# Performance work log

Hardware: AMD Instinct MI355X
Metric: run time of the kernel (lower is better)

## Reference

```python
import jax, jax.numpy as jnp
import numpy as np

E, T, H, I = 16, 4, 512, 1024  # expert_num, task_num, hidden_size, input_size
B = 8192


def setup_inputs() -> dict:
    key = jax.random.key(0)
    ks = jax.random.split(key, 8)
    s_i = 1.0 / np.sqrt(I)
    s_h = 1.0 / np.sqrt(H)
    return {
        "x": jax.random.normal(ks[0], (B, I), dtype=jnp.float32),
        "We": jax.random.uniform(ks[1], (E, H, I), jnp.float32, -s_i, s_i),
        "be": jax.random.uniform(ks[2], (E, H), jnp.float32, -s_i, s_i),
        "Wg": jax.random.uniform(ks[3], (T, E, I), jnp.float32, -s_i, s_i),
        "bg": jax.random.uniform(ks[4], (T, E), jnp.float32, -s_i, s_i),
        "Wf": jax.random.uniform(ks[5], (T, H), jnp.float32, -s_h, s_h),
        "bf": jax.random.uniform(ks[6], (T,), jnp.float32, -s_h, s_h),
    }


def reference(x, We, be, Wg, bg, Wf, bf):
    # expert outputs: relu(x @ We_e^T + be_e)  -> [B, E, H]
    eo = jax.nn.relu(jnp.einsum("bi,ehi->beh", x, We) + be[None])
    # gate outputs: softmax over experts        -> [B, T, E]
    g = jax.nn.softmax(jnp.einsum("bi,tei->bte", x, Wg) + bg[None], axis=-1)
    # gated combine                             -> [T, B, H]
    res = jnp.einsum("bte,beh->tbh", g, eo)
    # per-task scalar heads                     -> [T, B, 1]
    out = jnp.einsum("tbh,th->tb", res, Wf) + bf[:, None]
    return out[:, :, None]
```

## Files before the change

### kernel.cpp

```cpp
#include <hip/hip_runtime.h>
#include <hip/hip_bf16.h>
#include <stdint.h>


#define E_ 16
#define T_ 4
#define H_ 512
#define I_ 1024
#define B_ 8192
#define N_ (E_ * H_)
#define K_ I_

typedef __bf16 bf16x8 __attribute__((ext_vector_type(8)));
typedef float f32x4 __attribute__((ext_vector_type(4)));

__device__ __forceinline__ unsigned short f2bf_rne(float f) {
  unsigned int b = __float_as_uint(f);
  b += 0x7fffu + ((b >> 16) & 1u);
  return (unsigned short)(b >> 16);
}

#define N4X (B_ * K_ / 4)
#define N4W (N_ * K_ / 4)
#define N4G (64 * K_ / 4)

__global__ __launch_bounds__(256) void cvt3_kernel(const float* __restrict__ x,
                                                   const float* __restrict__ We,
                                                   const float* __restrict__ Wg,
                                                   const float* __restrict__ bfv,
                                                   unsigned short* __restrict__ xb,
                                                   unsigned short* __restrict__ wb,
                                                   unsigned short* __restrict__ wgb,
                                                   float* __restrict__ out) {
  int i = blockIdx.x * 256 + threadIdx.x;
  if (i < T_ * B_) out[i] = bfv[i >> 13];
  const float* src;
  unsigned short* dst;
  int j;
  if (i < N4X) {
    src = x; dst = xb; j = i;
  } else if (i < N4X + N4W) {
    src = We; dst = wb; j = i - N4X;
  } else if (i < N4X + N4W + N4G) {
    src = Wg; dst = wgb; j = i - (N4X + N4W);
  } else {
    return;
  }
  float4 v = reinterpret_cast<const float4*>(src)[j];
  ushort4 o;
  o.x = f2bf_rne(v.x);
  o.y = f2bf_rne(v.y);
  o.z = f2bf_rne(v.z);
  o.w = f2bf_rne(v.w);
  reinterpret_cast<ushort4*>(dst)[j] = o;
}

__device__ __forceinline__ void gld_lds16(const void* gp, void* lp) {
  __builtin_amdgcn_global_load_lds((const __attribute__((address_space(1))) void*)gp,
                                   (__attribute__((address_space(3))) void*)lp, 16, 0, 0);
}

__global__ __launch_bounds__(256) void logits_softmax_kernel(
    const unsigned short* __restrict__ A,
    const unsigned short* __restrict__ Bm,
    const float* __restrict__ bg,
    float* __restrict__ g)
{
  __shared__ struct {
    unsigned short A[128 * 32];
    unsigned short B[64 * 32];
  } st;

  const int tid = threadIdx.x;
  const int w = tid >> 6, l = tid & 63;
  const int m16 = l & 15, q = l >> 4;
  const size_t m0 = (size_t)blockIdx.x * 128;

  const int r0s = (w * 2 + 0) * 16 + (l >> 2);
  const int r1s = (w * 2 + 1) * 16 + (l >> 2);
  const int slot = l & 3;
  const int c0 = slot ^ ((r0s >> 1) & 3);
  const int c1 = slot ^ ((r1s >> 1) & 3);
  const size_t offA0 = (m0 + r0s) * K_ + c0 * 8;
  const size_t offA1 = (m0 + r1s) * K_ + c1 * 8;
  const int l0 = (w * 2 + 0) * 512;
  const int l1 = (w * 2 + 1) * 512;
  const int rBs = w * 16 + (l >> 2);
  const int cB = slot ^ ((rBs >> 1) & 3);
  const size_t offB = (size_t)rBs * K_ + cB * 8;
  const int lB = w * 512;

  const int arow = w * 32 + m16;
  const int sA = q ^ ((arow >> 1) & 3);
  const int sB = q ^ ((m16 >> 1) & 3);

  f32x4 acc[2][4] = {};

  for (int k0 = 0; k0 < K_; k0 += 32) {
    __syncthreads();
    gld_lds16(A + offA0 + k0, st.A + l0);
    gld_lds16(A + offA1 + k0, st.A + l1);
    gld_lds16(Bm + offB + k0, st.B + lB);
    __syncthreads();
    bf16x8 af[2], bfr[4];
#pragma unroll
    for (int i = 0; i < 2; ++i)
      af[i] = *reinterpret_cast<const bf16x8*>(st.A + (arow + i * 16) * 32 + sA * 8);
#pragma unroll
    for (int j = 0; j < 4; ++j)
      bfr[j] = *reinterpret_cast<const bf16x8*>(st.B + (j * 16 + m16) * 32 + sB * 8);
#pragma unroll
    for (int i = 0; i < 2; ++i)
#pragma unroll
      for (int j = 0; j < 4; ++j)
        acc[i][j] = __builtin_amdgcn_mfma_f32_16x16x32_bf16(af[i], bfr[j], acc[i][j], 0, 0, 0);
  }

  float bgv[4];
#pragma unroll
  for (int j = 0; j < 4; ++j) bgv[j] = bg[j * 16 + m16];

#pragma unroll
  for (int i = 0; i < 2; ++i) {
    float lg[4][4];
#pragma unroll
    for (int j = 0; j < 4; ++j)
#pragma unroll
      for (int r = 0; r < 4; ++r) lg[r][j] = acc[i][j][r] + bgv[j];
#pragma unroll
    for (int r = 0; r < 4; ++r) {
#pragma unroll
      for (int j = 0; j < 4; ++j) {
        float m = lg[r][j];
#pragma unroll
        for (int mask = 1; mask < 16; mask <<= 1) m = fmaxf(m, __shfl_xor(m, mask, 64));
        float ex = __expf(lg[r][j] - m);
        float s = ex;
#pragma unroll
        for (int mask = 1; mask < 16; mask <<= 1) s += __shfl_xor(s, mask, 64);
        size_t b = m0 + w * 32 + i * 16 + q * 4 + r;
        g[b * 64 + j * 16 + m16] = ex / s;
      }
    }
  }
}


extern __shared__ char smem[];

#define BARRIER()                          \
  do {                                     \
    asm volatile("" ::: "memory");         \
    __builtin_amdgcn_s_barrier();          \
    asm volatile("" ::: "memory");         \
  } while (0)
#define VMW(n) asm volatile("s_waitcnt vmcnt(" #n ")" ::: "memory")
#define LGKM0() asm volatile("s_waitcnt lgkmcnt(0)" ::: "memory")

#define STAGE4(t_)                                                             \
  do {                                                                         \
    const int bb_ = ((t_) & 3) * 32768;                                        \
    const int ko_ = (t_) * 32;                                                 \
    gld_lds16(A + baseAg + ko_, smem + bb_ + ldsW);                            \
    gld_lds16(A + baseAg + 16 * K_ + ko_, smem + bb_ + ldsW + 1024);           \
    gld_lds16(Bm + baseBg + ko_, smem + bb_ + 16384 + ldsW);                   \
    gld_lds16(Bm + baseBg + 16 * K_ + ko_, smem + bb_ + 16384 + ldsW + 1024);  \
  } while (0)

#define COMPUTE(t_)                                                                     \
  do {                                                                                  \
    const int bb_ = ((t_) & 3) * 32768;                                                 \
    bf16x8 af[8], bfr[4];                                                               \
    _Pragma("unroll") for (int i = 0; i < 8; ++i) af[i] =                               \
        *reinterpret_cast<const bf16x8*>(smem + bb_ + baseA_rd + i * 1024 + sl16);      \
    _Pragma("unroll") for (int j = 0; j < 4; ++j) bfr[j] =                              \
        *reinterpret_cast<const bf16x8*>(smem + bb_ + 16384 + baseB_rd + j * 1024 + sl16); \
    __builtin_amdgcn_s_setprio(1);                                                      \
    _Pragma("unroll") for (int i = 0; i < 8; ++i)                                       \
        _Pragma("unroll") for (int j = 0; j < 4; ++j)                                   \
            acc[i][j] = __builtin_amdgcn_mfma_f32_16x16x32_bf16(af[i], bfr[j],          \
                                                                acc[i][j], 0, 0, 0);   \
    __builtin_amdgcn_s_setprio(0);                                                      \
  } while (0)

__global__ __launch_bounds__(512, 2) void moe_main_kernel(
    const unsigned short* __restrict__ A,
    const unsigned short* __restrict__ Bm,
    const float* __restrict__ be,
    const float* __restrict__ Wf,
    const float* __restrict__ g,
    float* __restrict__ out)
{
  const int tid = threadIdx.x;
  const int w = tid >> 6, l = tid & 63;
  const int wm = w >> 2, wn = w & 3;
  const int m16 = l & 15, q = l >> 4;
  const int mb = blockIdx.x, nb = blockIdx.y;
  const size_t m0 = (size_t)mb * 256, n0 = (size_t)nb * 256;

  const int c8 = (((l & 3) ^ ((l >> 3) & 3)) * 8);
  const size_t baseAg = (m0 + w * 32 + (l >> 2)) * K_ + c8;
  const size_t baseBg = (n0 + w * 32 + (l >> 2)) * K_ + c8;
  const int ldsW = w * 2048;

  const int sl16 = (q ^ ((m16 >> 1) & 3)) * 16;
  const int baseA_rd = (wm * 128 + m16) * 64;
  const int baseB_rd = (wn * 64 + m16) * 64;

  f32x4 acc[8][4] = {};

  STAGE4(0);
  STAGE4(1);
  STAGE4(2);

#pragma unroll 1
  for (int t = 0; t < 29; ++t) {
    VMW(8);
    BARRIER();
    STAGE4(t + 3);
    COMPUTE(t);
    LGKM0();
  }
  VMW(8);
  BARRIER();
  COMPUTE(29);
  LGKM0();
  VMW(4);
  BARRIER();
  COMPUTE(30);
  LGKM0();
  VMW(0);
  BARRIER();
  COMPUTE(31);
  LGKM0();

  __syncthreads();

  float* allsums = (float*)smem;

  const int hb = (int)(n0 & 511);
  const int e_idx = (int)(n0 >> 9);

  float wfv[4][4];
#pragma unroll
  for (int t = 0; t < 4; ++t)
#pragma unroll
    for (int j = 0; j < 4; ++j)
      wfv[t][j] = Wf[t * H_ + hb + wn * 64 + j * 16 + m16];
  float bias[4];
#pragma unroll
  for (int j = 0; j < 4; ++j) bias[j] = be[n0 + wn * 64 + j * 16 + m16];

  const int b0s = m16 & 1, b1s = (m16 >> 1) & 1, b2s = (m16 >> 2) & 1, b3s = (m16 >> 3) & 1;
#pragma unroll
  for (int i = 0; i < 8; ++i) {
    float eo[4][4];
#pragma unroll
    for (int j = 0; j < 4; ++j)
#pragma unroll
      for (int r = 0; r < 4; ++r) eo[j][r] = fmaxf(acc[i][j][r] + bias[j], 0.f);
    float p[16];
#pragma unroll
    for (int r = 0; r < 4; ++r)
#pragma unroll
      for (int t = 0; t < 4; ++t) {
        float v = 0.f;
#pragma unroll
        for (int j = 0; j < 4; ++j) v += eo[j][r] * wfv[t][j];
        p[r * 4 + t] = v;
      }
    float q8[8];
#pragma unroll
    for (int m = 0; m < 8; ++m) {
      float sent = b0s ? p[2 * m] : p[2 * m + 1];
      float recv = __shfl_xor(sent, 1, 64);
      q8[m] = (b0s ? p[2 * m + 1] : p[2 * m]) + recv;
    }
    float q4[4];
#pragma unroll
    for (int u = 0; u < 4; ++u) {
      float sent = b1s ? q8[2 * u] : q8[2 * u + 1];
      float recv = __shfl_xor(sent, 2, 64);
      q4[u] = (b1s ? q8[2 * u + 1] : q8[2 * u]) + recv;
    }
    float q2[2];
#pragma unroll
    for (int u = 0; u < 2; ++u) {
      float sent = b2s ? q4[2 * u] : q4[2 * u + 1];
      float recv = __shfl_xor(sent, 4, 64);
      q2[u] = (b2s ? q4[2 * u + 1] : q4[2 * u]) + recv;
    }
    float sent = b3s ? q2[0] : q2[1];
    float recv = __shfl_xor(sent, 8, 64);
    float v = (b3s ? q2[1] : q2[0]) + recv;

    int row = wm * 128 + i * 16 + q * 4 + (m16 >> 2);
    allsums[wn * 1024 + row * 4 + (m16 & 3)] = v;
  }
  __syncthreads();

  {
    float2 s = *reinterpret_cast<float2*>(&allsums[0 * 1024 + tid * 2]);
    float2 x1 = *reinterpret_cast<float2*>(&allsums[1 * 1024 + tid * 2]);
    float2 x2 = *reinterpret_cast<float2*>(&allsums[2 * 1024 + tid * 2]);
    float2 x3 = *reinterpret_cast<float2*>(&allsums[3 * 1024 + tid * 2]);
    s.x += x1.x + x2.x + x3.x;
    s.y += x1.y + x2.y + x3.y;
#pragma unroll
    for (int oi = 0; oi < 2; ++oi) {
      int o = tid * 2 + oi;
      int row = o >> 2, t = o & 3;
      float sv = oi ? s.y : s.x;
      size_t b = m0 + row;
      float gv = g[b * 64 + t * 16 + e_idx];
      atomicAdd(&out[(size_t)t * B_ + b], gv * sv);
    }
  }
}

extern "C" void kernel_launch(void* const* d_in, const int* in_sizes, int n_in,
                              void* d_out, int out_size, void* d_ws, size_t ws_size,
                              hipStream_t stream) {
  const float* x = (const float*)d_in[0];
  const float* We = (const float*)d_in[1];
  const float* be = (const float*)d_in[2];
  const float* Wg = (const float*)d_in[3];
  const float* bg = (const float*)d_in[4];
  const float* Wf = (const float*)d_in[5];
  const float* bf = (const float*)d_in[6];
  float* out = (float*)d_out;

  unsigned short* xb = (unsigned short*)d_ws;
  unsigned short* wb = xb + (size_t)B_ * K_;
  unsigned short* wgb = wb + (size_t)N_ * K_;
  float* g = (float*)(wgb + (size_t)64 * K_);

  hipFuncSetAttribute((const void*)moe_main_kernel,
                      hipFuncAttributeMaxDynamicSharedMemorySize, 131072);

  cvt3_kernel<<<(N4X + N4W + N4G + 255) / 256, 256, 0, stream>>>(x, We, Wg, bf, xb, wb, wgb, out);
  logits_softmax_kernel<<<B_ / 128, 256, 0, stream>>>(xb, wgb, bg, g);
  dim3 grid(B_ / 256, N_ / 256);
  moe_main_kernel<<<grid, 512, 131072, stream>>>(xb, wb, be, Wf, g, out);
}
```

Baseline: 259.4 us.

## Double-buffer LDS fragment registers to overlap reads with MFMA

Splits the per-tile compute into a fragment-read step and an MFMA step, and keeps two register sets of A/B fragments. Reads for tile t+1 are issued while the MFMAs for tile t run, and the main loop is unrolled by two to alternate the sets. The global-load wait is relaxed to vmcnt(4) to match the new schedule, and scheduling barriers pin the order. The cost is another full set of fragment registers, which under the current launch bounds could cause spills or lower occupancy.

After: 253.5 us. 2.3% less time.

```diff
diff --git a/kernel.cpp b/kernel.cpp
--- a/kernel.cpp
+++ b/kernel.cpp
@@ -156,6 +156,7 @@
   } while (0)
 #define VMW(n) asm volatile("s_waitcnt vmcnt(" #n ")" ::: "memory")
 #define LGKM0() asm volatile("s_waitcnt lgkmcnt(0)" ::: "memory")
+#define SCHED0() __builtin_amdgcn_sched_barrier(0)
 
 #define STAGE4(t_)                                                             \
   do {                                                                         \
@@ -167,20 +168,23 @@
     gld_lds16(Bm + baseBg + 16 * K_ + ko_, smem + bb_ + 16384 + ldsW + 1024);  \
   } while (0)
 
-#define COMPUTE(t_)                                                                     \
-  do {                                                                                  \
-    const int bb_ = ((t_) & 3) * 32768;                                                 \
-    bf16x8 af[8], bfr[4];                                                               \
-    _Pragma("unroll") for (int i = 0; i < 8; ++i) af[i] =                               \
-        *reinterpret_cast<const bf16x8*>(smem + bb_ + baseA_rd + i * 1024 + sl16);      \
-    _Pragma("unroll") for (int j = 0; j < 4; ++j) bfr[j] =                              \
-        *reinterpret_cast<const bf16x8*>(smem + bb_ + 16384 + baseB_rd + j * 1024 + sl16); \
-    __builtin_amdgcn_s_setprio(1);                                                      \
-    _Pragma("unroll") for (int i = 0; i < 8; ++i)                                       \
-        _Pragma("unroll") for (int j = 0; j < 4; ++j)                                   \
-            acc[i][j] = __builtin_amdgcn_mfma_f32_16x16x32_bf16(af[i], bfr[j],          \
-                                                                acc[i][j], 0, 0, 0);   \
-    __builtin_amdgcn_s_setprio(0);                                                      \
+#define READF(S, t_)                                                                      \
+  do {                                                                                    \
+    const int bb_ = ((t_) & 3) * 32768;                                                   \
+    _Pragma("unroll") for (int i = 0; i < 8; ++i) af##S[i] =                              \
+        *reinterpret_cast<const bf16x8*>(smem + bb_ + baseA_rd + i * 1024 + sl16);        \
+    _Pragma("unroll") for (int j = 0; j < 4; ++j) bfr##S[j] =                             \
+        *reinterpret_cast<const bf16x8*>(smem + bb_ + 16384 + baseB_rd + j * 1024 + sl16);\
+  } while (0)
+
+#define MFMA32(S)                                                                         \
+  do {                                                                                    \
+    __builtin_amdgcn_s_setprio(1);                                                        \
+    _Pragma("unroll") for (int i = 0; i < 8; ++i)                                         \
+        _Pragma("unroll") for (int j = 0; j < 4; ++j)                                     \
+            acc[i][j] = __builtin_amdgcn_mfma_f32_16x16x32_bf16(af##S[i], bfr##S[j],      \
+                                                                acc[i][j], 0, 0, 0);      \
+    __builtin_amdgcn_s_setprio(0);                                                        \
   } while (0)
 
 __global__ __launch_bounds__(512, 2) void moe_main_kernel(
@@ -208,31 +212,54 @@
   const int baseB_rd = (wn * 64 + m16) * 64;
 
   f32x4 acc[8][4] = {};
+  bf16x8 afA[8], bfrA[4], afB[8], bfrB[4];
 
   STAGE4(0);
   STAGE4(1);
   STAGE4(2);
+  VMW(8);
+  BARRIER();
+  READF(A, 0);
+  LGKM0();
+  SCHED0();
 
 #pragma unroll 1
-  for (int t = 0; t < 29; ++t) {
-    VMW(8);
+  for (int t = 0; t < 28; t += 2) {
+    VMW(4);
     BARRIER();
     STAGE4(t + 3);
-    COMPUTE(t);
+    READF(B, t + 1);
+    MFMA32(A);
     LGKM0();
-  }
-  VMW(8);
-  BARRIER();
-  COMPUTE(29);
-  LGKM0();
+    SCHED0();
+    VMW(4);
+    BARRIER();
+    STAGE4(t + 4);
+    READF(A, t + 2);
+    MFMA32(B);
+    LGKM0();
+    SCHED0();
+  }
   VMW(4);
   BARRIER();
-  COMPUTE(30);
+  STAGE4(31);
+  READF(B, 29);
+  MFMA32(A);
   LGKM0();
+  SCHED0();
+  VMW(4);
+  BARRIER();
+  READF(A, 30);
+  MFMA32(B);
+  LGKM0();
+  SCHED0();
   VMW(0);
   BARRIER();
-  COMPUTE(31);
+  READF(B, 31);
+  MFMA32(A);
   LGKM0();
+  SCHED0();
+  MFMA32(B);
 
   __syncthreads();
 
```
